# Optimization experiments

Hardware: AMD Instinct MI355X
Metric: run time of the kernel (lower is better)

Reference implementation:

```python
import jax, jax.numpy as jnp
import numpy as np
from jax import lax

# Hyperparameters (mirror init_kwargs)
R = 0.2          # ball-query radius
K = 32           # max neighbors per ball
SPATIAL_STRIDE = 4
TKS = 3          # temporal kernel size (odd)
TSTRIDE = 1
PAD = (1, 1)     # replicate temporal padding


def fps(xyz, m):
    """Furthest point sampling. xyz: (N,3) -> (m,) int32 indices. Starts at index 0."""
    N = xyz.shape[0]

    def body(carry, _):
        dists, last = carry
        d = jnp.sum((xyz - xyz[last]) ** 2, axis=-1)
        dists = jnp.minimum(dists, d)
        nxt = jnp.argmax(dists).astype(jnp.int32)
        return (dists, nxt), nxt

    init = (jnp.full((N,), 1e10, xyz.dtype), jnp.int32(0))
    _, idx = lax.scan(body, init, None, length=m - 1)
    return jnp.concatenate([jnp.zeros((1,), jnp.int32), idx])


def ball_query(pts, anchors):
    """pts: (N,3), anchors: (M,3) -> (M,K) int32. First K indices within radius R,
    padded with the first found index (0 if the ball is empty) -- pointnet2 semantics."""
    N = pts.shape[0]
    d2 = jnp.sum((anchors[:, None, :] - pts[None, :, :]) ** 2, axis=-1)  # (M,N)
    score = jnp.where(d2 < R * R, jnp.arange(N, dtype=jnp.int32)[None, :], N)
    vals, _ = lax.top_k(-score, K)          # ascending first-K valid indices
    sel = -vals                              # (M,K)
    first = sel[:, :1]
    sel = jnp.where(sel >= N, first, sel)    # pad with first in-ball index
    sel = jnp.where(sel >= N, 0, sel)        # empty ball -> index 0
    return sel


def setup_inputs() -> dict:
    key = jax.random.key(0)
    k1, k2, k3, k4, k5 = jax.random.split(key, 5)
    B, T, N, Cin = 4, 8, 4096, 64
    C0, C1 = 64, 128
    xyzs = jax.random.uniform(k1, (B, T, N, 3), dtype=jnp.float32)
    features = jax.random.normal(k2, (B, T, Cin, N), dtype=jnp.float32)
    Wd = jax.random.normal(k3, (C0, 4), dtype=jnp.float32) * 0.1    # conv_d 1x1 weight
    Wf = jax.random.normal(k4, (C0, Cin), dtype=jnp.float32) * 0.1  # conv_f 1x1 weight
    W1 = jax.random.normal(k5, (C1, C0), dtype=jnp.float32) * 0.1   # mlp 1x1 weight
    return {"xyzs": xyzs, "features": features, "Wd": Wd, "Wf": Wf, "W1": W1}


def reference(xyzs, features, Wd, Wf, W1):
    B, T, N, _ = xyzs.shape
    M = N // SPATIAL_STRIDE
    half = TKS // 2
    # replicate temporal padding (PAD = (1,1))
    xp = jnp.concatenate([xyzs[:, :1], xyzs, xyzs[:, -1:]], axis=1)          # (B,L,N,3)
    fp = jnp.concatenate([features[:, :1], features, features[:, -1:]], axis=1)  # (B,L,C,N)
    L = T + PAD[0] + PAD[1]

    new_xyzs, new_feats = [], []
    for t in range(half, L - half, TSTRIDE):
        aidx = jax.vmap(lambda p: fps(p, M))(xp[:, t])                       # (B,M)
        anchor = jnp.take_along_axis(xp[:, t], aidx[:, :, None], axis=1)    # (B,M,3)
        acc = None
        for i in range(t - half, t + half + 1):
            pts = xp[:, i]                                                   # (B,N,3)
            idx = jax.vmap(ball_query)(pts, anchor)                          # (B,M,K)
            grouped = jax.vmap(lambda p, ii: p[ii])(pts, idx)                # (B,M,K,3)
            disp = grouped - anchor[:, :, None, :]
            tcol = jnp.full(disp.shape[:-1] + (1,), float(i - t), disp.dtype)
            d4 = jnp.concatenate([disp, tcol], axis=-1)                      # (B,M,K,4)
            dfeat = jax.nn.relu(jnp.einsum('bmkc,oc->bmko', d4, Wd))         # conv_d
            gf = jax.vmap(lambda f, ii: f.T[ii])(fp[:, i], idx)              # (B,M,K,Cin)
            ffeat = jax.nn.relu(jnp.einsum('bmkc,oc->bmko', gf, Wf))         # conv_f
            feat = ffeat + dfeat                                             # operator '+'
            feat = jax.nn.relu(jnp.einsum('bmkc,oc->bmko', feat, W1))        # mlp
            feat = jnp.max(feat, axis=2)                                     # spatial max -> (B,M,C1)
            acc = feat if acc is None else acc + feat                        # temporal sum
        new_xyzs.append(anchor)
        new_feats.append(jnp.transpose(acc, (0, 2, 1)))                      # (B,C1,M)
    return jnp.stack(new_xyzs, axis=1), jnp.stack(new_feats, axis=1)
```

## Files before the change

kernel.cpp:

```cpp
#include <hip/hip_runtime.h>
#include <hip/hip_bf16.h>

constexpr int B = 4, T = 8, N = 4096, C0 = 64, C1 = 128;
constexpr int M = 1024, KNN = 32;

typedef __attribute__((ext_vector_type(8))) short short8;
typedef __attribute__((ext_vector_type(4))) float f32x4;

__device__ __forceinline__ unsigned short f2bf(float x) {
  unsigned u = __float_as_uint(x);
  u = u + 0x7FFFu + ((u >> 16) & 1u);
  return (unsigned short)(u >> 16);
}
__device__ __forceinline__ float bf2f(unsigned short h) {
  return __uint_as_float((unsigned)h << 16);
}
__device__ __forceinline__ short f2bf_rn(float x) {
  union { __hip_bfloat16 b; unsigned short u; } v;
  v.b = __float2bfloat16(x);
  return (short)v.u;
}

template <int CTRL>
__device__ __forceinline__ float dppf(float x) {
  return __int_as_float(__builtin_amdgcn_update_dpp(0, __float_as_int(x), CTRL, 0xF, 0xF, true));
}
template <int CTRL>
__device__ __forceinline__ int dppi(int x) {
  return __builtin_amdgcn_update_dpp(0, x, CTRL, 0xF, 0xF, true);
}
template <int CTRL>
__device__ __forceinline__ unsigned long long dppu64(unsigned long long x) {
  unsigned lo = (unsigned)dppi<CTRL>((int)(unsigned)x);
  unsigned hi = (unsigned)dppi<CTRL>((int)(unsigned)(x >> 32));
  return ((unsigned long long)hi << 32) | lo;
}
__device__ __forceinline__ void kmerge(unsigned long long& a, unsigned long long b) {
  if (b > a) a = b;
}
__device__ __forceinline__ unsigned long long kmax(unsigned long long a, unsigned long long b) {
  return b > a ? b : a;
}

__global__ __launch_bounds__(256) void prep_wft(const float* __restrict__ Wf,
                                                float* __restrict__ WfT) {
  int t = blockIdx.x * 256 + threadIdx.x;
  if (t < 64 * 64) WfT[t] = Wf[(t & 63) * 64 + (t >> 6)];
}

__global__ __launch_bounds__(256) void prep_w1frag(const float* __restrict__ W1,
                                                   unsigned short* __restrict__ w1hi,
                                                   unsigned short* __restrict__ w1lo) {
  int t = blockIdx.x * 256 + threadIdx.x;
  if (t >= 8192) return;
  int j = t & 7, lane = (t >> 3) & 63, mt = (t >> 9) & 7, kt = t >> 12;
  int row = mt * 16 + (lane & 15);
  int k = kt * 32 + (lane >> 4) * 8 + j;
  float v = W1[row * 64 + k];
  unsigned short hi = f2bf(v);
  w1hi[t] = hi;
  w1lo[t] = f2bf(v - bf2f(hi));
}

__device__ void fps_body(char* smem, const float* __restrict__ xyz,
                         float* __restrict__ out_xyz, int bt) {
  float4* P4 = (float4*)smem;
  int* pick_l = (int*)(smem + 65536);
  unsigned long long* wslot = (unsigned long long*)(smem + 65536 + 4096);
  const float* p = xyz + (size_t)bt * N * 3;
  int tid = threadIdx.x;
  int lane = tid & 63, w = tid >> 6;
  for (int i = tid; i < N; i += 256)
    P4[i] = make_float4(p[i * 3 + 0], p[i * 3 + 1], p[i * 3 + 2], 0.f);
  if (tid == 0) pick_l[0] = 0;
  __syncthreads();
  float X[16], Y[16], Z[16], D[16];
  unsigned inv[16];
#pragma unroll
  for (int j = 0; j < 16; ++j) {
    float4 v = P4[j * 256 + tid];
    X[j] = v.x; Y[j] = v.y; Z[j] = v.z;
    D[j] = 1e10f;
    inv[j] = ~(unsigned)(j * 256 + tid);
  }
  int lidx = 0;
  for (int s = 1; s < M; ++s) {
    float4 lp = P4[lidx];
    unsigned long long k[16];
#pragma unroll
    for (int j = 0; j < 16; ++j) {
      float dx = __fsub_rn(X[j], lp.x);
      float dy = __fsub_rn(Y[j], lp.y);
      float dz = __fsub_rn(Z[j], lp.z);
      float d = __fadd_rn(__fadd_rn(__fmul_rn(dx, dx), __fmul_rn(dy, dy)), __fmul_rn(dz, dz));
      float nd = fminf(D[j], d);
      D[j] = nd;
      k[j] = ((unsigned long long)__float_as_uint(nd) << 32) | inv[j];
    }
#pragma unroll
    for (int st = 8; st >= 1; st >>= 1)
#pragma unroll
      for (int j = 0; j < st; ++j) kmerge(k[j], k[j + st]);
    unsigned long long best = k[0];
    kmerge(best, dppu64<0xB1>(best));
    kmerge(best, dppu64<0x4E>(best));
    kmerge(best, dppu64<0x141>(best));
    kmerge(best, dppu64<0x140>(best));
    int buf = s & 1;
    if ((lane & 15) == 0) wslot[buf * 16 + w * 4 + (lane >> 4)] = best;
    __syncthreads();
    const ulonglong2* ws2 = (const ulonglong2*)&wslot[buf * 16];
    ulonglong2 a0 = ws2[0], a1 = ws2[1], a2 = ws2[2], a3 = ws2[3];
    ulonglong2 a4 = ws2[4], a5 = ws2[5], a6 = ws2[6], a7 = ws2[7];
    unsigned long long t0 = kmax(kmax(a0.x, a0.y), kmax(a1.x, a1.y));
    unsigned long long t1 = kmax(kmax(a2.x, a2.y), kmax(a3.x, a3.y));
    unsigned long long t2 = kmax(kmax(a4.x, a4.y), kmax(a5.x, a5.y));
    unsigned long long t3 = kmax(kmax(a6.x, a6.y), kmax(a7.x, a7.y));
    unsigned long long g = kmax(kmax(t0, t1), kmax(t2, t3));
    lidx = (int)(~(unsigned)g);
    if (tid == 0) pick_l[s] = lidx;
  }
  __syncthreads();
  float* outp = out_xyz + (size_t)bt * M * 3;
  for (int mm = tid; mm < M; mm += 256) {
    float4 v = P4[pick_l[mm]];
    outp[mm * 3 + 0] = v.x;
    outp[mm * 3 + 1] = v.y;
    outp[mm * 3 + 2] = v.z;
  }
}

__device__ void rff_body(char* smem, const float* __restrict__ f,
                         const float* __restrict__ WfT, unsigned short* __restrict__ RFFh,
                         int rid) {
  float (*tile)[65] = (float (*)[65])smem;
  int bt = rid >> 6;
  int n0 = (rid & 63) * 64;
  const float* src = f + (size_t)bt * C0 * N;
  int tx = threadIdx.x & 63, ty = threadIdx.x >> 6;
  for (int r = ty; r < 64; r += 4)
    tile[r][tx] = src[(size_t)r * N + n0 + tx];
  __syncthreads();
  float acc[16];
#pragma unroll
  for (int oo = 0; oo < 16; ++oo) acc[oo] = 0.f;
  int obase = ty * 16;
#pragma unroll 4
  for (int c = 0; c < 64; ++c) {
    float fv = tile[c][tx];
    const float* wr = WfT + c * 64 + obase;
#pragma unroll
    for (int oo = 0; oo < 16; ++oo) acc[oo] = fmaf(fv, wr[oo], acc[oo]);
  }
  __syncthreads();
#pragma unroll
  for (int oo = 0; oo < 16; ++oo) tile[obase + oo][tx] = fmaxf(acc[oo], 0.f);
  __syncthreads();
  unsigned short* dst = RFFh + ((size_t)bt * N + n0) * 64;
  for (int r = ty; r < 64; r += 4)
    dst[(size_t)r * 64 + tx] = f2bf(tile[tx][r]);
}

__global__ __launch_bounds__(256) void fps_rff_kernel(const float* __restrict__ xyz,
                                                      float* __restrict__ out_xyz,
                                                      const float* __restrict__ feats,
                                                      const float* __restrict__ WfT,
                                                      unsigned short* __restrict__ RFFh) {
  __shared__ __align__(16) char smem[65536 + 4096 + 256];
  if (blockIdx.x < 32)
    fps_body(smem, xyz, out_xyz, blockIdx.x);
  else
    rff_body(smem, feats, WfT, RFFh, blockIdx.x - 32);
}

__global__ __launch_bounds__(256) void ballq_kernel(const float* __restrict__ xyz,
                                                    const float* __restrict__ anchors,
                                                    int* __restrict__ idxbuf) {
  const float R2 = 0.04f;
  int w = threadIdx.x >> 6, lane = threadIdx.x & 63;
  int q = blockIdx.x * 4 + w;
  int m = q & (M - 1);
  int di = (q >> 10) % 3;
  int bt = q / (M * 3);
  int b = bt >> 3, t = bt & 7;
  int srct = t + di - 1;
  srct = srct < 0 ? 0 : (srct > 7 ? 7 : srct);
  const float* anc = anchors + ((size_t)(bt * M + m)) * 3;
  float ax = anc[0], ay = anc[1], az = anc[2];
  const float* pts = xyz + ((size_t)(b * T + srct)) * N * 3;
  int* outp = idxbuf + (size_t)q * KNN;
  int cnt = 0, first = 0;
  for (int c = 0; c < N / 64 && cnt < KNN; ++c) {
    int pi = c * 64 + lane;
    const float* pp = pts + (size_t)pi * 3;
    float dx = __fsub_rn(ax, pp[0]);
    float dy = __fsub_rn(ay, pp[1]);
    float dz = __fsub_rn(az, pp[2]);
    float d2 = __fadd_rn(__fadd_rn(__fmul_rn(dx, dx), __fmul_rn(dy, dy)), __fmul_rn(dz, dz));
    bool hit = d2 < R2;
    unsigned long long mask = __ballot(hit);
    if (cnt == 0 && mask) first = c * 64 + (int)__builtin_ctzll(mask);
    int prefix = (int)__popcll(mask & ((1ull << lane) - 1ull));
    int slot = cnt + prefix;
    if (hit && slot < KNN) outp[slot] = pi;
    cnt += (int)__popcll(mask);
  }
  int cntK = cnt < KNN ? cnt : KNN;
  int fill = (cnt == 0) ? 0 : first;
  if (lane < KNN && lane >= cntK) outp[lane] = fill;
}

__global__ __launch_bounds__(256) void mlp_kernel(const float* __restrict__ xyz,
                                                  const unsigned short* __restrict__ RFFh,
                                                  const unsigned short* __restrict__ w1hi,
                                                  const unsigned short* __restrict__ w1lo,
                                                  const float* __restrict__ Wd,
                                                  const float* __restrict__ anchors,
                                                  const int* __restrict__ idxbuf,
                                                  float* __restrict__ out_feats) {
  __shared__ unsigned short Ah[8192];
  __shared__ unsigned short Al[8192];
  __shared__ float wd_l[256];
  __shared__ float fstage[4][128];
  int tid = threadIdx.x;
  {
    uint4* dh = (uint4*)Ah;
    const uint4* sh = (const uint4*)w1hi;
    uint4* dl = (uint4*)Al;
    const uint4* sl = (const uint4*)w1lo;
    for (int i = tid; i < 1024; i += 256) { dh[i] = sh[i]; dl[i] = sl[i]; }
    wd_l[tid] = Wd[tid];
  }
  __syncthreads();
  int w = tid >> 6, lane = tid & 63;
  int nloc = lane & 15, grp = lane >> 4;
  int bid = blockIdx.x;
  int swz = ((bid & 7) << 10) | (bid >> 3);
  int bt = swz >> 8;
  int m0 = (swz & 255) * 4;
  int m = m0 + w;
  int b = bt >> 3, t = bt & 7;
  int aoff = __builtin_amdgcn_readfirstlane(bt * M + m);
  float ax = anchors[(size_t)aoff * 3 + 0];
  float ay = anchors[(size_t)aoff * 3 + 1];
  float az = anchors[(size_t)aoff * 3 + 2];
  f32x4 acc[8];
#pragma unroll
  for (int mt = 0; mt < 8; ++mt) acc[mt] = (f32x4){0.f, 0.f, 0.f, 0.f};

  short8 pg0[2][2], pg1[2][2];
  float ppx[2][2], ppy[2][2], ppz[2][2];

#define MLOADP(BUF, DI)                                                        \
  {                                                                            \
    int srct = t + (DI)-1;                                                     \
    srct = srct < 0 ? 0 : (srct > 7 ? 7 : srct);                               \
    const unsigned short* rf = RFFh + ((size_t)(b * T + srct)) * N * 64;       \
    const float* pts = xyz + ((size_t)(b * T + srct)) * N * 3;                 \
    const int* ip = idxbuf + ((size_t)((bt * 3 + (DI)) * M + m)) * KNN;        \
    int n0 = ip[nloc], n1 = ip[16 + nloc];                                     \
    _Pragma("unroll") for (int kt = 0; kt < 2; ++kt) {                         \
      pg0[BUF][kt] = *(const short8*)(rf + (size_t)n0 * 64 + kt * 32 + grp * 8); \
      pg1[BUF][kt] = *(const short8*)(rf + (size_t)n1 * 64 + kt * 32 + grp * 8); \
    }                                                                          \
    ppx[BUF][0] = pts[n0 * 3 + 0];                                             \
    ppy[BUF][0] = pts[n0 * 3 + 1];                                             \
    ppz[BUF][0] = pts[n0 * 3 + 2];                                             \
    ppx[BUF][1] = pts[n1 * 3 + 0];                                             \
    ppy[BUF][1] = pts[n1 * 3 + 1];                                             \
    ppz[BUF][1] = pts[n1 * 3 + 2];                                             \
  }

#define MCOMPUTE(BUF, DI)                                                      \
  {                                                                            \
    int zro = 0;                                                               \
    asm volatile("" : "+v"(zro));                                              \
    const unsigned short* AhO = Ah + zro;                                      \
    const unsigned short* AlO = Al + zro;                                      \
    const float* wdO = (const float*)wd_l + zro;                               \
    float tvv = (float)((DI)-1);                                               \
    float dx0 = ppx[BUF][0] - ax, dy0 = ppy[BUF][0] - ay, dz0 = ppz[BUF][0] - az; \
    float dx1 = ppx[BUF][1] - ax, dy1 = ppy[BUF][1] - ay, dz1 = ppz[BUF][1] - az; \
    short8 Bh[2][2];                                             \
    _Pragma("unroll") for (int kt = 0; kt < 2; ++kt) {                         \
      short8 bh0, bh1;                                                         \
      _Pragma("unroll") for (int j = 0; j < 8; ++j) {                          \
        int ch = kt * 32 + grp * 8 + j;                                        \
        float4 wr = *(const float4*)&wdO[ch * 4];                              \
        float dd0 = fmaf(dx0, wr.x, fmaf(dy0, wr.y, fmaf(dz0, wr.z, tvv * wr.w))); \
        float dd1 = fmaf(dx1, wr.x, fmaf(dy1, wr.y, fmaf(dz1, wr.z, tvv * wr.w))); \
        float h0 = bf2f((unsigned short)pg0[BUF][kt][j]) + fmaxf(dd0, 0.f);    \
        float h1 = bf2f((unsigned short)pg1[BUF][kt][j]) + fmaxf(dd1, 0.f);    \
        bh0[j] = f2bf_rn(h0);                                                  \
        bh1[j] = f2bf_rn(h1);                                                  \
      }                                                                        \
      Bh[kt][0] = bh0;                                                         \
      Bh[kt][1] = bh1;                                                         \
    }                                                                          \
    _Pragma("unroll") for (int hf = 0; hf < 2; ++hf) {                         \
      f32x4 c[4][2];                                                           \
      _Pragma("unroll") for (int mq = 0; mq < 4; ++mq) {                       \
        c[mq][0] = (f32x4){0.f, 0.f, 0.f, 0.f};                                \
        c[mq][1] = (f32x4){0.f, 0.f, 0.f, 0.f};                                \
      }                                                                        \
      _Pragma("unroll") for (int kt = 0; kt < 2; ++kt) {                       \
        _Pragma("unroll") for (int mq = 0; mq < 4; ++mq) {                     \
          int fo = ((kt * 8 + hf * 4 + mq) * 64 + lane) * 8;                   \
          short8 ahf = *(const short8*)&AhO[fo];                               \
          short8 alf = *(const short8*)&AlO[fo];                               \
          c[mq][0] =                                                           \
              __builtin_amdgcn_mfma_f32_16x16x32_bf16(ahf, Bh[kt][0], c[mq][0], 0, 0, 0); \
          c[mq][0] =                                                           \
              __builtin_amdgcn_mfma_f32_16x16x32_bf16(alf, Bh[kt][0], c[mq][0], 0, 0, 0); \
          c[mq][1] =                                                           \
              __builtin_amdgcn_mfma_f32_16x16x32_bf16(ahf, Bh[kt][1], c[mq][1], 0, 0, 0); \
          c[mq][1] =                                                           \
              __builtin_amdgcn_mfma_f32_16x16x32_bf16(alf, Bh[kt][1], c[mq][1], 0, 0, 0); \
        }                                                                      \
      }                                                                        \
      _Pragma("unroll") for (int mq = 0; mq < 4; ++mq)                         \
          _Pragma("unroll") for (int r = 0; r < 4; ++r) {                      \
        float o = fmaxf(c[mq][0][r], c[mq][1][r]);                             \
        o = fmaxf(o, dppf<0xB1>(o));                                           \
        o = fmaxf(o, dppf<0x4E>(o));                                           \
        o = fmaxf(o, dppf<0x141>(o));                                          \
        o = fmaxf(o, dppf<0x140>(o));                                          \
        acc[hf * 4 + mq][r] += fmaxf(o, 0.f);                                  \
      }                                                                        \
    }                                                                          \
  }

  MLOADP(0, 0)
  MLOADP(1, 1)
  MCOMPUTE(0, 0)
  MLOADP(0, 2)
  MCOMPUTE(1, 1)
  MCOMPUTE(0, 2)
#undef MLOADP
#undef MCOMPUTE

  if (nloc == 0) {
#pragma unroll
    for (int mt = 0; mt < 8; ++mt)
#pragma unroll
      for (int r = 0; r < 4; ++r)
        fstage[w][mt * 16 + grp * 4 + r] = acc[mt][r];
  }
  __syncthreads();
  if (tid < 128) {
    float4 v = make_float4(fstage[0][tid], fstage[1][tid], fstage[2][tid], fstage[3][tid]);
    *(float4*)&out_feats[((size_t)(bt * C1 + tid)) * M + m0] = v;
  }
}

extern "C" void kernel_launch(void* const* d_in, const int* in_sizes, int n_in,
                              void* d_out, int out_size, void* d_ws, size_t ws_size,
                              hipStream_t stream) {
  const float* xyzs = (const float*)d_in[0];
  const float* feats = (const float*)d_in[1];
  const float* Wd = (const float*)d_in[2];
  const float* Wf = (const float*)d_in[3];
  const float* W1 = (const float*)d_in[4];
  float* out_xyz = (float*)d_out;
  float* out_feats = (float*)d_out + (size_t)B * T * M * 3;
  char* ws = (char*)d_ws;
  unsigned short* RFFh = (unsigned short*)ws;
  int* idxbuf = (int*)(ws + (size_t)B * T * N * 64 * 4);
  char* tail = ws + (size_t)B * T * N * 64 * 4 + (size_t)B * T * 3 * M * KNN * 4;
  float* WfT = (float*)tail;
  unsigned short* w1hi = (unsigned short*)(tail + 16384);
  unsigned short* w1lo = (unsigned short*)(tail + 32768);
  prep_wft<<<16, 256, 0, stream>>>(Wf, WfT);
  prep_w1frag<<<32, 256, 0, stream>>>(W1, w1hi, w1lo);
  fps_rff_kernel<<<32 + 2048, 256, 0, stream>>>(xyzs, out_xyz, feats, WfT, RFFh);
  ballq_kernel<<<(B * T * 3 * M) / 4, 256, 0, stream>>>(xyzs, out_xyz, idxbuf);
  mlp_kernel<<<(B * T * M) / 4, 256, 0, stream>>>(xyzs, RFFh, w1hi, w1lo, Wd, out_xyz,
                                                  idxbuf, out_feats);
}
```

Before: 1.056 ms.

## Fuse FPS, ball query and MLP into persistent producer-consumer megakernel

FPS blocks now publish anchors incrementally and bump a per-frame progress counter with release stores. 480 persistent consumer blocks spin on that counter, run the ball query inline into LDS and then do the MLP, so consumers overlap with the serial FPS. This also removes the idxbuf round trip through global memory. RFF moves to its own kernel ahead of the megakernel, and the FPS reduction is trimmed to a full-wave DPP reduction and a 4-slot barrier, which lowers per-iteration sync cost. The risks are spin-wait correctness (it depends on all 32 FPS blocks being co-resident) and reduced consumer parallelism.

```diff
diff --git a/kernel.cpp b/kernel.cpp
--- a/kernel.cpp
+++ b/kernel.cpp
@@ -3,6 +3,9 @@
 
 constexpr int B = 4, T = 8, N = 4096, C0 = 64, C1 = 128;
 constexpr int M = 1024, KNN = 32;
+constexpr int NCONS = 480;
+constexpr int NBLK = 32 + NCONS;
+constexpr int SMEM_BYTES = 49408;
 
 typedef __attribute__((ext_vector_type(8))) short short8;
 typedef __attribute__((ext_vector_type(4))) float f32x4;
@@ -40,6 +43,19 @@
 }
 __device__ __forceinline__ unsigned long long kmax(unsigned long long a, unsigned long long b) {
   return b > a ? b : a;
+}
+
+__device__ __forceinline__ void aStoreF(float* p, float v) {
+  __hip_atomic_store(p, v, __ATOMIC_RELAXED, __HIP_MEMORY_SCOPE_AGENT);
+}
+__device__ __forceinline__ float aLoadF(const float* p) {
+  return __hip_atomic_load(p, __ATOMIC_RELAXED, __HIP_MEMORY_SCOPE_AGENT);
+}
+__device__ __forceinline__ void aStoreRelI(int* p, int v) {
+  __hip_atomic_store(p, v, __ATOMIC_RELEASE, __HIP_MEMORY_SCOPE_AGENT);
+}
+__device__ __forceinline__ int aLoadAcqI(const int* p) {
+  return __hip_atomic_load(p, __ATOMIC_ACQUIRE, __HIP_MEMORY_SCOPE_AGENT);
 }
 
 __global__ __launch_bounds__(256) void prep_wft(const float* __restrict__ Wf,
@@ -62,36 +78,86 @@
   w1lo[t] = f2bf(v - bf2f(hi));
 }
 
+__global__ __launch_bounds__(256) void rff_kernel(const float* __restrict__ f,
+                                                  const float* __restrict__ WfT,
+                                                  unsigned short* __restrict__ RFFh) {
+  __shared__ float tile[64][65];
+  int bt = blockIdx.y;
+  int n0 = blockIdx.x * 64;
+  const float* src = f + (size_t)bt * C0 * N;
+  int tx = threadIdx.x & 63, ty = threadIdx.x >> 6;
+  for (int r = ty; r < 64; r += 4)
+    tile[r][tx] = src[(size_t)r * N + n0 + tx];
+  __syncthreads();
+  float acc[16];
+#pragma unroll
+  for (int oo = 0; oo < 16; ++oo) acc[oo] = 0.f;
+  int obase = ty * 16;
+#pragma unroll 4
+  for (int c = 0; c < 64; ++c) {
+    float fv = tile[c][tx];
+    const float* wr = WfT + c * 64 + obase;
+#pragma unroll
+    for (int oo = 0; oo < 16; ++oo) acc[oo] = fmaf(fv, wr[oo], acc[oo]);
+  }
+  __syncthreads();
+#pragma unroll
+  for (int oo = 0; oo < 16; ++oo) tile[obase + oo][tx] = fmaxf(acc[oo], 0.f);
+  __syncthreads();
+  unsigned short* dst = RFFh + ((size_t)bt * N + n0) * 64;
+  for (int r = ty; r < 64; r += 4)
+    dst[(size_t)r * 64 + tx] = f2bf(tile[tx][r]);
+}
+
 __device__ void fps_body(char* smem, const float* __restrict__ xyz,
-                         float* __restrict__ out_xyz, int bt) {
-  float4* P4 = (float4*)smem;
-  int* pick_l = (int*)(smem + 65536);
-  unsigned long long* wslot = (unsigned long long*)(smem + 65536 + 4096);
+                         float* __restrict__ anchors, int* __restrict__ progress, int bt) {
+  float* xs = (float*)smem;
+  float* ys = xs + N;
+  float* zs = ys + N;
+  unsigned long long* wslot = (unsigned long long*)(smem + 49152);
   const float* p = xyz + (size_t)bt * N * 3;
   int tid = threadIdx.x;
   int lane = tid & 63, w = tid >> 6;
-  for (int i = tid; i < N; i += 256)
-    P4[i] = make_float4(p[i * 3 + 0], p[i * 3 + 1], p[i * 3 + 2], 0.f);
-  if (tid == 0) pick_l[0] = 0;
+  for (int i = tid; i < N; i += 256) {
+    xs[i] = p[i * 3 + 0];
+    ys[i] = p[i * 3 + 1];
+    zs[i] = p[i * 3 + 2];
+  }
   __syncthreads();
   float X[16], Y[16], Z[16], D[16];
   unsigned inv[16];
 #pragma unroll
   for (int j = 0; j < 16; ++j) {
-    float4 v = P4[j * 256 + tid];
-    X[j] = v.x; Y[j] = v.y; Z[j] = v.z;
+    X[j] = xs[j * 256 + tid];
+    Y[j] = ys[j * 256 + tid];
+    Z[j] = zs[j * 256 + tid];
     D[j] = 1e10f;
     inv[j] = ~(unsigned)(j * 256 + tid);
   }
+  if (tid == 0) {
+    float* a0 = anchors + (size_t)bt * M * 3;
+    aStoreF(a0 + 0, xs[0]);
+    aStoreF(a0 + 1, ys[0]);
+    aStoreF(a0 + 2, zs[0]);
+  }
   int lidx = 0;
   for (int s = 1; s < M; ++s) {
-    float4 lp = P4[lidx];
+    float lx = xs[lidx], ly = ys[lidx], lz = zs[lidx];
+    if (tid == 0) {
+      if (s > 1) {
+        float* ap = anchors + ((size_t)(bt * M + s - 1)) * 3;
+        aStoreF(ap + 0, lx);
+        aStoreF(ap + 1, ly);
+        aStoreF(ap + 2, lz);
+      }
+      if ((s & 31) == 0) aStoreRelI(&progress[bt], s);
+    }
     unsigned long long k[16];
 #pragma unroll
     for (int j = 0; j < 16; ++j) {
-      float dx = __fsub_rn(X[j], lp.x);
-      float dy = __fsub_rn(Y[j], lp.y);
-      float dz = __fsub_rn(Z[j], lp.z);
+      float dx = __fsub_rn(X[j], lx);
+      float dy = __fsub_rn(Y[j], ly);
+      float dz = __fsub_rn(Z[j], lz);
       float d = __fadd_rn(__fadd_rn(__fmul_rn(dx, dx), __fmul_rn(dy, dy)), __fmul_rn(dz, dz));
       float nd = fminf(D[j], d);
       D[j] = nd;
@@ -106,89 +172,31 @@
     kmerge(best, dppu64<0x4E>(best));
     kmerge(best, dppu64<0x141>(best));
     kmerge(best, dppu64<0x140>(best));
+    kmerge(best, dppu64<0x142>(best));
+    kmerge(best, dppu64<0x143>(best));
     int buf = s & 1;
-    if ((lane & 15) == 0) wslot[buf * 16 + w * 4 + (lane >> 4)] = best;
-    __syncthreads();
-    const ulonglong2* ws2 = (const ulonglong2*)&wslot[buf * 16];
-    ulonglong2 a0 = ws2[0], a1 = ws2[1], a2 = ws2[2], a3 = ws2[3];
-    ulonglong2 a4 = ws2[4], a5 = ws2[5], a6 = ws2[6], a7 = ws2[7];
-    unsigned long long t0 = kmax(kmax(a0.x, a0.y), kmax(a1.x, a1.y));
-    unsigned long long t1 = kmax(kmax(a2.x, a2.y), kmax(a3.x, a3.y));
-    unsigned long long t2 = kmax(kmax(a4.x, a4.y), kmax(a5.x, a5.y));
-    unsigned long long t3 = kmax(kmax(a6.x, a6.y), kmax(a7.x, a7.y));
-    unsigned long long g = kmax(kmax(t0, t1), kmax(t2, t3));
+    if (lane == 63) wslot[buf * 4 + w] = best;
+    asm volatile("s_waitcnt lgkmcnt(0)" ::: "memory");
+    __builtin_amdgcn_s_barrier();
+    __builtin_amdgcn_sched_barrier(0);
+    const ulonglong2* ws2 = (const ulonglong2*)&wslot[buf * 4];
+    ulonglong2 a0 = ws2[0], a1 = ws2[1];
+    unsigned long long g = kmax(kmax(a0.x, a0.y), kmax(a1.x, a1.y));
     lidx = (int)(~(unsigned)g);
-    if (tid == 0) pick_l[s] = lidx;
-  }
-  __syncthreads();
-  float* outp = out_xyz + (size_t)bt * M * 3;
-  for (int mm = tid; mm < M; mm += 256) {
-    float4 v = P4[pick_l[mm]];
-    outp[mm * 3 + 0] = v.x;
-    outp[mm * 3 + 1] = v.y;
-    outp[mm * 3 + 2] = v.z;
-  }
-}
-
-__device__ void rff_body(char* smem, const float* __restrict__ f,
-                         const float* __restrict__ WfT, unsigned short* __restrict__ RFFh,
-                         int rid) {
-  float (*tile)[65] = (float (*)[65])smem;
-  int bt = rid >> 6;
-  int n0 = (rid & 63) * 64;
-  const float* src = f + (size_t)bt * C0 * N;
-  int tx = threadIdx.x & 63, ty = threadIdx.x >> 6;
-  for (int r = ty; r < 64; r += 4)
-    tile[r][tx] = src[(size_t)r * N + n0 + tx];
-  __syncthreads();
-  float acc[16];
-#pragma unroll
-  for (int oo = 0; oo < 16; ++oo) acc[oo] = 0.f;
-  int obase = ty * 16;
-#pragma unroll 4
-  for (int c = 0; c < 64; ++c) {
-    float fv = tile[c][tx];
-    const float* wr = WfT + c * 64 + obase;
-#pragma unroll
-    for (int oo = 0; oo < 16; ++oo) acc[oo] = fmaf(fv, wr[oo], acc[oo]);
-  }
-  __syncthreads();
-#pragma unroll
-  for (int oo = 0; oo < 16; ++oo) tile[obase + oo][tx] = fmaxf(acc[oo], 0.f);
-  __syncthreads();
-  unsigned short* dst = RFFh + ((size_t)bt * N + n0) * 64;
-  for (int r = ty; r < 64; r += 4)
-    dst[(size_t)r * 64 + tx] = f2bf(tile[tx][r]);
-}
-
-__global__ __launch_bounds__(256) void fps_rff_kernel(const float* __restrict__ xyz,
-                                                      float* __restrict__ out_xyz,
-                                                      const float* __restrict__ feats,
-                                                      const float* __restrict__ WfT,
-                                                      unsigned short* __restrict__ RFFh) {
-  __shared__ __align__(16) char smem[65536 + 4096 + 256];
-  if (blockIdx.x < 32)
-    fps_body(smem, xyz, out_xyz, blockIdx.x);
-  else
-    rff_body(smem, feats, WfT, RFFh, blockIdx.x - 32);
-}
-
-__global__ __launch_bounds__(256) void ballq_kernel(const float* __restrict__ xyz,
-                                                    const float* __restrict__ anchors,
-                                                    int* __restrict__ idxbuf) {
+  }
+  if (tid == 0) {
+    float* ap = anchors + ((size_t)(bt * M + M - 1)) * 3;
+    aStoreF(ap + 0, xs[lidx]);
+    aStoreF(ap + 1, ys[lidx]);
+    aStoreF(ap + 2, zs[lidx]);
+    aStoreRelI(&progress[bt], M);
+  }
+}
+
+__device__ void ballq_one(const float* __restrict__ pts, float ax, float ay, float az,
+                          int* outp) {
   const float R2 = 0.04f;
-  int w = threadIdx.x >> 6, lane = threadIdx.x & 63;
-  int q = blockIdx.x * 4 + w;
-  int m = q & (M - 1);
-  int di = (q >> 10) % 3;
-  int bt = q / (M * 3);
-  int b = bt >> 3, t = bt & 7;
-  int srct = t + di - 1;
-  srct = srct < 0 ? 0 : (srct > 7 ? 7 : srct);
-  const float* anc = anchors + ((size_t)(bt * M + m)) * 3;
-  float ax = anc[0], ay = anc[1], az = anc[2];
-  const float* pts = xyz + ((size_t)(b * T + srct)) * N * 3;
-  int* outp = idxbuf + (size_t)q * KNN;
+  int lane = threadIdx.x & 63;
   int cnt = 0, first = 0;
   for (int c = 0; c < N / 64 && cnt < KNN; ++c) {
     int pi = c * 64 + lane;
@@ -210,19 +218,21 @@
   if (lane < KNN && lane >= cntK) outp[lane] = fill;
 }
 
-__global__ __launch_bounds__(256) void mlp_kernel(const float* __restrict__ xyz,
-                                                  const unsigned short* __restrict__ RFFh,
-                                                  const unsigned short* __restrict__ w1hi,
-                                                  const unsigned short* __restrict__ w1lo,
-                                                  const float* __restrict__ Wd,
-                                                  const float* __restrict__ anchors,
-                                                  const int* __restrict__ idxbuf,
-                                                  float* __restrict__ out_feats) {
-  __shared__ unsigned short Ah[8192];
-  __shared__ unsigned short Al[8192];
-  __shared__ float wd_l[256];
-  __shared__ float fstage[4][128];
+__device__ void consumer_body(char* smem, const float* __restrict__ xyz,
+                              const float* __restrict__ anchors,
+                              const unsigned short* __restrict__ RFFh,
+                              const unsigned short* __restrict__ w1hi,
+                              const unsigned short* __restrict__ w1lo,
+                              const float* __restrict__ Wd,
+                              float* __restrict__ out_feats,
+                              int* __restrict__ progress, int cid) {
   int tid = threadIdx.x;
+  unsigned short* Ah = (unsigned short*)smem;
+  unsigned short* Al = (unsigned short*)(smem + 16384);
+  float* wd_l = (float*)(smem + 32768);
+  float* anc_lds = (float*)(smem + 33792);
+  int* idx_lds = (int*)(smem + 33856);
+  float (*fstage)[128] = (float (*)[128])(smem + 35392);
   {
     uint4* dh = (uint4*)Ah;
     const uint4* sh = (const uint4*)w1hi;
@@ -234,123 +244,159 @@
   __syncthreads();
   int w = tid >> 6, lane = tid & 63;
   int nloc = lane & 15, grp = lane >> 4;
-  int bid = blockIdx.x;
-  int swz = ((bid & 7) << 10) | (bid >> 3);
-  int bt = swz >> 8;
-  int m0 = (swz & 255) * 4;
-  int m = m0 + w;
-  int b = bt >> 3, t = bt & 7;
-  int aoff = __builtin_amdgcn_readfirstlane(bt * M + m);
-  float ax = anchors[(size_t)aoff * 3 + 0];
-  float ay = anchors[(size_t)aoff * 3 + 1];
-  float az = anchors[(size_t)aoff * 3 + 2];
-  f32x4 acc[8];
-#pragma unroll
-  for (int mt = 0; mt < 8; ++mt) acc[mt] = (f32x4){0.f, 0.f, 0.f, 0.f};
-
-  short8 pg0[2][2], pg1[2][2];
-  float ppx[2][2], ppy[2][2], ppz[2][2];
-
-#define MLOADP(BUF, DI)                                                        \
-  {                                                                            \
-    int srct = t + (DI)-1;                                                     \
-    srct = srct < 0 ? 0 : (srct > 7 ? 7 : srct);                               \
-    const unsigned short* rf = RFFh + ((size_t)(b * T + srct)) * N * 64;       \
-    const float* pts = xyz + ((size_t)(b * T + srct)) * N * 3;                 \
-    const int* ip = idxbuf + ((size_t)((bt * 3 + (DI)) * M + m)) * KNN;        \
-    int n0 = ip[nloc], n1 = ip[16 + nloc];                                     \
-    _Pragma("unroll") for (int kt = 0; kt < 2; ++kt) {                         \
+  for (int tile = cid; tile < 8192; tile += NCONS) {
+    int mg = tile >> 5, bt = tile & 31;
+    int m0 = mg * 4;
+    int b = bt >> 3, t = bt & 7;
+    int m = m0 + w;
+    if (tid == 0) {
+      for (int it = 0; it < 1000000 && aLoadAcqI(&progress[bt]) < m0 + 4; ++it)
+        __builtin_amdgcn_s_sleep(8);
+    }
+    __syncthreads();
+    if (lane == 0) {
+      const float* ap = anchors + ((size_t)(bt * M + m)) * 3;
+      anc_lds[w * 4 + 0] = aLoadF(ap + 0);
+      anc_lds[w * 4 + 1] = aLoadF(ap + 1);
+      anc_lds[w * 4 + 2] = aLoadF(ap + 2);
+    }
+    asm volatile("s_waitcnt lgkmcnt(0)" ::: "memory");
+    __builtin_amdgcn_sched_barrier(0);
+    float ax = anc_lds[w * 4 + 0];
+    float ay = anc_lds[w * 4 + 1];
+    float az = anc_lds[w * 4 + 2];
+    for (int di = 0; di < 3; ++di) {
+      int srct = t + di - 1;
+      srct = srct < 0 ? 0 : (srct > 7 ? 7 : srct);
+      ballq_one(xyz + ((size_t)(b * T + srct)) * N * 3, ax, ay, az,
+                idx_lds + (w * 3 + di) * KNN);
+    }
+    asm volatile("s_waitcnt lgkmcnt(0)" ::: "memory");
+    __builtin_amdgcn_sched_barrier(0);
+    f32x4 acc[8];
+#pragma unroll
+    for (int mt = 0; mt < 8; ++mt) acc[mt] = (f32x4){0.f, 0.f, 0.f, 0.f};
+    short8 pg0[2][2], pg1[2][2];
+    float ppx[2][2], ppy[2][2], ppz[2][2];
+
+#define MLOADP(BUF, DI)                                                          \
+  {                                                                              \
+    int srct = t + (DI)-1;                                                       \
+    srct = srct < 0 ? 0 : (srct > 7 ? 7 : srct);                                 \
+    const unsigned short* rf = RFFh + ((size_t)(b * T + srct)) * N * 64;         \
+    const float* pts = xyz + ((size_t)(b * T + srct)) * N * 3;                   \
+    const int* ipw = idx_lds + (w * 3 + (DI)) * KNN;                             \
+    int n0 = ipw[nloc], n1 = ipw[16 + nloc];                                     \
+    _Pragma("unroll") for (int kt = 0; kt < 2; ++kt) {                           \
       pg0[BUF][kt] = *(const short8*)(rf + (size_t)n0 * 64 + kt * 32 + grp * 8); \
       pg1[BUF][kt] = *(const short8*)(rf + (size_t)n1 * 64 + kt * 32 + grp * 8); \
-    }                                                                          \
-    ppx[BUF][0] = pts[n0 * 3 + 0];                                             \
-    ppy[BUF][0] = pts[n0 * 3 + 1];                                             \
-    ppz[BUF][0] = pts[n0 * 3 + 2];                                             \
-    ppx[BUF][1] = pts[n1 * 3 + 0];                                             \
-    ppy[BUF][1] = pts[n1 * 3 + 1];                                             \
-    ppz[BUF][1] = pts[n1 * 3 + 2];                                             \
-  }
-
-#define MCOMPUTE(BUF, DI)                                                      \
-  {                                                                            \
-    int zro = 0;                                                               \
-    asm volatile("" : "+v"(zro));                                              \
-    const unsigned short* AhO = Ah + zro;                                      \
-    const unsigned short* AlO = Al + zro;                                      \
-    const float* wdO = (const float*)wd_l + zro;                               \
-    float tvv = (float)((DI)-1);                                               \
-    float dx0 = ppx[BUF][0] - ax, dy0 = ppy[BUF][0] - ay, dz0 = ppz[BUF][0] - az; \
-    float dx1 = ppx[BUF][1] - ax, dy1 = ppy[BUF][1] - ay, dz1 = ppz[BUF][1] - az; \
-    short8 Bh[2][2];                                             \
-    _Pragma("unroll") for (int kt = 0; kt < 2; ++kt) {                         \
-      short8 bh0, bh1;                                                         \
-      _Pragma("unroll") for (int j = 0; j < 8; ++j) {                          \
-        int ch = kt * 32 + grp * 8 + j;                                        \
-        float4 wr = *(const float4*)&wdO[ch * 4];                              \
+    }                                                                            \
+    ppx[BUF][0] = pts[n0 * 3 + 0];                                               \
+    ppy[BUF][0] = pts[n0 * 3 + 1];                                               \
+    ppz[BUF][0] = pts[n0 * 3 + 2];                                               \
+    ppx[BUF][1] = pts[n1 * 3 + 0];                                               \
+    ppy[BUF][1] = pts[n1 * 3 + 1];                                               \
+    ppz[BUF][1] = pts[n1 * 3 + 2];                                               \
+  }
+
+#define MCOMPUTE(BUF, DI)                                                          \
+  {                                                                                \
+    int zro = 0;                                                                   \
+    asm volatile("" : "+v"(zro));                                                  \
+    const unsigned short* AhO = Ah + zro;                                          \
+    const unsigned short* AlO = Al + zro;                                          \
+    const float* wdO = wd_l + zro;                                                 \
+    float tvv = (float)((DI)-1);                                                   \
+    float dx0 = ppx[BUF][0] - ax, dy0 = ppy[BUF][0] - ay, dz0 = ppz[BUF][0] - az;  \
+    float dx1 = ppx[BUF][1] - ax, dy1 = ppy[BUF][1] - ay, dz1 = ppz[BUF][1] - az;  \
+    short8 Bh[2][2];                                                               \
+    _Pragma("unroll") for (int kt = 0; kt < 2; ++kt) {                             \
+      short8 bh0, bh1;                                                             \
+      _Pragma("unroll") for (int j = 0; j < 8; ++j) {                              \
+        int ch = kt * 32 + grp * 8 + j;                                            \
+        float4 wr = *(const float4*)&wdO[ch * 4];                                  \
         float dd0 = fmaf(dx0, wr.x, fmaf(dy0, wr.y, fmaf(dz0, wr.z, tvv * wr.w))); \
         float dd1 = fmaf(dx1, wr.x, fmaf(dy1, wr.y, fmaf(dz1, wr.z, tvv * wr.w))); \
-        float h0 = bf2f((unsigned short)pg0[BUF][kt][j]) + fmaxf(dd0, 0.f);    \
-        float h1 = bf2f((unsigned short)pg1[BUF][kt][j]) + fmaxf(dd1, 0.f);    \
-        bh0[j] = f2bf_rn(h0);                                                  \
-        bh1[j] = f2bf_rn(h1);                                                  \
-      }                                                                        \
-      Bh[kt][0] = bh0;                                                         \
-      Bh[kt][1] = bh1;                                                         \
-    }                                                                          \
-    _Pragma("unroll") for (int hf = 0; hf < 2; ++hf) {                         \
-      f32x4 c[4][2];                                                           \
-      _Pragma("unroll") for (int mq = 0; mq < 4; ++mq) {                       \
-        c[mq][0] = (f32x4){0.f, 0.f, 0.f, 0.f};                                \
-        c[mq][1] = (f32x4){0.f, 0.f, 0.f, 0.f};                                \
-      }                                                                        \
-      _Pragma("unroll") for (int kt = 0; kt < 2; ++kt) {                       \
-        _Pragma("unroll") for (int mq = 0; mq < 4; ++mq) {                     \
-          int fo = ((kt * 8 + hf * 4 + mq) * 64 + lane) * 8;                   \
-          short8 ahf = *(const short8*)&AhO[fo];                               \
-          short8 alf = *(const short8*)&AlO[fo];                               \
-          c[mq][0] =                                                           \
-              __builtin_amdgcn_mfma_f32_16x16x32_bf16(ahf, Bh[kt][0], c[mq][0], 0, 0, 0); \
-          c[mq][0] =                                                           \
-              __builtin_amdgcn_mfma_f32_16x16x32_bf16(alf, Bh[kt][0], c[mq][0], 0, 0, 0); \
-          c[mq][1] =                                                           \
-              __builtin_amdgcn_mfma_f32_16x16x32_bf16(ahf, Bh[kt][1], c[mq][1], 0, 0, 0); \
-          c[mq][1] =                                                           \
-              __builtin_amdgcn_mfma_f32_16x16x32_bf16(alf, Bh[kt][1], c[mq][1], 0, 0, 0); \
-        }                                                                      \
-      }                                                                        \
-      _Pragma("unroll") for (int mq = 0; mq < 4; ++mq)                         \
-          _Pragma("unroll") for (int r = 0; r < 4; ++r) {                      \
-        float o = fmaxf(c[mq][0][r], c[mq][1][r]);                             \
-        o = fmaxf(o, dppf<0xB1>(o));                                           \
-        o = fmaxf(o, dppf<0x4E>(o));                                           \
-        o = fmaxf(o, dppf<0x141>(o));                                          \
-        o = fmaxf(o, dppf<0x140>(o));                                          \
-        acc[hf * 4 + mq][r] += fmaxf(o, 0.f);                                  \
-      }                                                                        \
-    }                                                                          \
-  }
-
-  MLOADP(0, 0)
-  MLOADP(1, 1)
-  MCOMPUTE(0, 0)
-  MLOADP(0, 2)
-  MCOMPUTE(1, 1)
-  MCOMPUTE(0, 2)
+        float h0 = bf2f((unsigned short)pg0[BUF][kt][j]) + fmaxf(dd0, 0.f);        \
+        float h1 = bf2f((unsigned short)pg1[BUF][kt][j]) + fmaxf(dd1, 0.f);        \
+        bh0[j] = f2bf_rn(h0);                                                      \
+        bh1[j] = f2bf_rn(h1);                                                      \
+      }                                                                            \
+      Bh[kt][0] = bh0;                                                             \
+      Bh[kt][1] = bh1;                                                             \
+    }                                                                              \
+    _Pragma("unroll") for (int hf = 0; hf < 2; ++hf) {                             \
+      f32x4 c[4][2];                                                               \
+      _Pragma("unroll") for (int mq = 0; mq < 4; ++mq) {                           \
+        c[mq][0] = (f32x4){0.f, 0.f, 0.f, 0.f};                                    \
+        c[mq][1] = (f32x4){0.f, 0.f, 0.f, 0.f};                                    \
+      }                                                                            \
+      _Pragma("unroll") for (int kt = 0; kt < 2; ++kt) {                           \
+        _Pragma("unroll") for (int mq = 0; mq < 4; ++mq) {                         \
+          int fo = ((kt * 8 + hf * 4 + mq) * 64 + lane) * 8;                       \
+          short8 ahf = *(const short8*)&AhO[fo];                                   \
+          short8 alf = *(const short8*)&AlO[fo];                                   \
+          c[mq][0] = __builtin_amdgcn_mfma_f32_16x16x32_bf16(ahf, Bh[kt][0],       \
+                                                             c[mq][0], 0, 0, 0);  \
+          c[mq][0] = __builtin_amdgcn_mfma_f32_16x16x32_bf16(alf, Bh[kt][0],       \
+                                                             c[mq][0], 0, 0, 0);  \
+          c[mq][1] = __builtin_amdgcn_mfma_f32_16x16x32_bf16(ahf, Bh[kt][1],       \
+                                                             c[mq][1], 0, 0, 0);  \
+          c[mq][1] = __builtin_amdgcn_mfma_f32_16x16x32_bf16(alf, Bh[kt][1],       \
+                                                             c[mq][1], 0, 0, 0);  \
+        }                                                                          \
+      }                                                                            \
+      _Pragma("unroll") for (int mq = 0; mq < 4; ++mq)                             \
+          _Pragma("unroll") for (int r = 0; r < 4; ++r) {                          \
+        float o = fmaxf(c[mq][0][r], c[mq][1][r]);                                 \
+        o = fmaxf(o, dppf<0xB1>(o));                                               \
+        o = fmaxf(o, dppf<0x4E>(o));                                               \
+        o = fmaxf(o, dppf<0x141>(o));                                              \
+        o = fmaxf(o, dppf<0x140>(o));                                              \
+        acc[hf * 4 + mq][r] += fmaxf(o, 0.f);                                      \
+      }                                                                            \
+    }                                                                              \
+  }
+
+    MLOADP(0, 0)
+    MLOADP(1, 1)
+    MCOMPUTE(0, 0)
+    MLOADP(0, 2)
+    MCOMPUTE(1, 1)
+    MCOMPUTE(0, 2)
 #undef MLOADP
 #undef MCOMPUTE
 
-  if (nloc == 0) {
-#pragma unroll
-    for (int mt = 0; mt < 8; ++mt)
-#pragma unroll
-      for (int r = 0; r < 4; ++r)
-        fstage[w][mt * 16 + grp * 4 + r] = acc[mt][r];
-  }
-  __syncthreads();
-  if (tid < 128) {
-    float4 v = make_float4(fstage[0][tid], fstage[1][tid], fstage[2][tid], fstage[3][tid]);
-    *(float4*)&out_feats[((size_t)(bt * C1 + tid)) * M + m0] = v;
-  }
+    if (nloc == 0) {
+#pragma unroll
+      for (int mt = 0; mt < 8; ++mt)
+#pragma unroll
+        for (int r = 0; r < 4; ++r)
+          fstage[w][mt * 16 + grp * 4 + r] = acc[mt][r];
+    }
+    __syncthreads();
+    if (tid < 128) {
+      float4 v = make_float4(fstage[0][tid], fstage[1][tid], fstage[2][tid], fstage[3][tid]);
+      *(float4*)&out_feats[((size_t)(bt * C1 + tid)) * M + m0] = v;
+    }
+    __syncthreads();
+  }
+}
+
+__global__ __launch_bounds__(256) void mega_kernel(const float* __restrict__ xyz,
+                                                   float* __restrict__ anchors,
+                                                   const unsigned short* __restrict__ RFFh,
+                                                   const unsigned short* __restrict__ w1hi,
+                                                   const unsigned short* __restrict__ w1lo,
+                                                   const float* __restrict__ Wd,
+                                                   float* __restrict__ out_feats,
+                                                   int* __restrict__ progress) {
+  __shared__ __align__(16) char smem[SMEM_BYTES];
+  if (blockIdx.x < 32)
+    fps_body(smem, xyz, anchors, progress, blockIdx.x);
+  else
+    consumer_body(smem, xyz, anchors, RFFh, w1hi, w1lo, Wd, out_feats, progress,
+                  blockIdx.x - 32);
 }
 
 extern "C" void kernel_launch(void* const* d_in, const int* in_sizes, int n_in,
@@ -365,15 +411,15 @@
   float* out_feats = (float*)d_out + (size_t)B * T * M * 3;
   char* ws = (char*)d_ws;
   unsigned short* RFFh = (unsigned short*)ws;
-  int* idxbuf = (int*)(ws + (size_t)B * T * N * 64 * 4);
-  char* tail = ws + (size_t)B * T * N * 64 * 4 + (size_t)B * T * 3 * M * KNN * 4;
+  char* tail = ws + (size_t)B * T * N * 64 * 2;
   float* WfT = (float*)tail;
   unsigned short* w1hi = (unsigned short*)(tail + 16384);
   unsigned short* w1lo = (unsigned short*)(tail + 32768);
+  int* progress = (int*)(tail + 49152);
+  hipMemsetAsync(progress, 0, 128, stream);
   prep_wft<<<16, 256, 0, stream>>>(Wf, WfT);
   prep_w1frag<<<32, 256, 0, stream>>>(W1, w1hi, w1lo);
-  fps_rff_kernel<<<32 + 2048, 256, 0, stream>>>(xyzs, out_xyz, feats, WfT, RFFh);
-  ballq_kernel<<<(B * T * 3 * M) / 4, 256, 0, stream>>>(xyzs, out_xyz, idxbuf);
-  mlp_kernel<<<(B * T * M) / 4, 256, 0, stream>>>(xyzs, RFFh, w1hi, w1lo, Wd, out_xyz,
-                                                  idxbuf, out_feats);
-}
+  rff_kernel<<<dim3(N / 64, B * T), 256, 0, stream>>>(feats, WfT, RFFh);
+  mega_kernel<<<NBLK, 256, 0, stream>>>(xyzs, out_xyz, RFFh, w1hi, w1lo, Wd, out_feats,
+                                        progress);
+}
```

New measurement: 1.293 ms. 1.22x slower.

## Speed up FPS loop with packed math, wave-wide reduction and lighter barrier

Applied to the files above, without the earlier changes.

The FPS distance update now uses two-wide float vectors so the compiler can emit packed FP32 ops, and point coordinates move to SoA shared arrays. Each wave finishes its argmax with extra row-broadcast DPP steps so only one lane per wave writes to LDS. The block sync becomes a raw s_barrier with a waitcnt, which cuts the per-iteration cross-wave reduction from 16 slots to 4. Picked anchors are written straight to global memory inside the loop, and the LDS footprint and workspace offset are shrunk. FPS is a serial chain of 1023 steps, so per-step latency matters; the raw barrier gives up the compiler's fence guarantees, and fp contract is disabled to keep rounding identical.

```diff
diff --git a/kernel.cpp b/kernel.cpp
--- a/kernel.cpp
+++ b/kernel.cpp
@@ -6,6 +6,7 @@
 
 typedef __attribute__((ext_vector_type(8))) short short8;
 typedef __attribute__((ext_vector_type(4))) float f32x4;
+typedef __attribute__((ext_vector_type(2))) float f32x2;
 
 __device__ __forceinline__ unsigned short f2bf(float x) {
   unsigned u = __float_as_uint(x);
@@ -64,38 +65,55 @@
 
 __device__ void fps_body(char* smem, const float* __restrict__ xyz,
                          float* __restrict__ out_xyz, int bt) {
-  float4* P4 = (float4*)smem;
-  int* pick_l = (int*)(smem + 65536);
-  unsigned long long* wslot = (unsigned long long*)(smem + 65536 + 4096);
+#pragma clang fp contract(off)
+  float* xs = (float*)smem;
+  float* ys = xs + N;
+  float* zs = ys + N;
+  unsigned long long* wslot = (unsigned long long*)(smem + 49152);
   const float* p = xyz + (size_t)bt * N * 3;
   int tid = threadIdx.x;
   int lane = tid & 63, w = tid >> 6;
-  for (int i = tid; i < N; i += 256)
-    P4[i] = make_float4(p[i * 3 + 0], p[i * 3 + 1], p[i * 3 + 2], 0.f);
-  if (tid == 0) pick_l[0] = 0;
-  __syncthreads();
-  float X[16], Y[16], Z[16], D[16];
+  for (int i = tid; i < N; i += 256) {
+    xs[i] = p[i * 3 + 0];
+    ys[i] = p[i * 3 + 1];
+    zs[i] = p[i * 3 + 2];
+  }
+  __syncthreads();
+  f32x2 X2[8], Y2[8], Z2[8], D2[8];
   unsigned inv[16];
 #pragma unroll
-  for (int j = 0; j < 16; ++j) {
-    float4 v = P4[j * 256 + tid];
-    X[j] = v.x; Y[j] = v.y; Z[j] = v.z;
-    D[j] = 1e10f;
-    inv[j] = ~(unsigned)(j * 256 + tid);
+  for (int j = 0; j < 8; ++j) {
+    int i0 = (2 * j) * 256 + tid, i1 = (2 * j + 1) * 256 + tid;
+    X2[j] = (f32x2){xs[i0], xs[i1]};
+    Y2[j] = (f32x2){ys[i0], ys[i1]};
+    Z2[j] = (f32x2){zs[i0], zs[i1]};
+    D2[j] = (f32x2){1e10f, 1e10f};
+    inv[2 * j] = ~(unsigned)i0;
+    inv[2 * j + 1] = ~(unsigned)i1;
+  }
+  if (tid == 0) {
+    float* a0 = out_xyz + (size_t)bt * M * 3;
+    a0[0] = xs[0]; a0[1] = ys[0]; a0[2] = zs[0];
   }
   int lidx = 0;
   for (int s = 1; s < M; ++s) {
-    float4 lp = P4[lidx];
+    float lx = xs[lidx], ly = ys[lidx], lz = zs[lidx];
+    if (tid == 0 && s > 1) {
+      float* ap = out_xyz + ((size_t)(bt * M + s - 1)) * 3;
+      ap[0] = lx; ap[1] = ly; ap[2] = lz;
+    }
+    f32x2 l2x = (f32x2){lx, lx}, l2y = (f32x2){ly, ly}, l2z = (f32x2){lz, lz};
     unsigned long long k[16];
 #pragma unroll
-    for (int j = 0; j < 16; ++j) {
-      float dx = __fsub_rn(X[j], lp.x);
-      float dy = __fsub_rn(Y[j], lp.y);
-      float dz = __fsub_rn(Z[j], lp.z);
-      float d = __fadd_rn(__fadd_rn(__fmul_rn(dx, dx), __fmul_rn(dy, dy)), __fmul_rn(dz, dz));
-      float nd = fminf(D[j], d);
-      D[j] = nd;
-      k[j] = ((unsigned long long)__float_as_uint(nd) << 32) | inv[j];
+    for (int j = 0; j < 8; ++j) {
+      f32x2 dx = X2[j] - l2x;
+      f32x2 dy = Y2[j] - l2y;
+      f32x2 dz = Z2[j] - l2z;
+      f32x2 d = dx * dx + dy * dy + dz * dz;
+      f32x2 nd = __builtin_elementwise_min(D2[j], d);
+      D2[j] = nd;
+      k[2 * j] = ((unsigned long long)__float_as_uint(nd.x) << 32) | inv[2 * j];
+      k[2 * j + 1] = ((unsigned long long)__float_as_uint(nd.y) << 32) | inv[2 * j + 1];
     }
 #pragma unroll
     for (int st = 8; st >= 1; st >>= 1)
@@ -106,27 +124,21 @@
     kmerge(best, dppu64<0x4E>(best));
     kmerge(best, dppu64<0x141>(best));
     kmerge(best, dppu64<0x140>(best));
+    kmerge(best, dppu64<0x142>(best));
+    kmerge(best, dppu64<0x143>(best));
     int buf = s & 1;
-    if ((lane & 15) == 0) wslot[buf * 16 + w * 4 + (lane >> 4)] = best;
-    __syncthreads();
-    const ulonglong2* ws2 = (const ulonglong2*)&wslot[buf * 16];
-    ulonglong2 a0 = ws2[0], a1 = ws2[1], a2 = ws2[2], a3 = ws2[3];
-    ulonglong2 a4 = ws2[4], a5 = ws2[5], a6 = ws2[6], a7 = ws2[7];
-    unsigned long long t0 = kmax(kmax(a0.x, a0.y), kmax(a1.x, a1.y));
-    unsigned long long t1 = kmax(kmax(a2.x, a2.y), kmax(a3.x, a3.y));
-    unsigned long long t2 = kmax(kmax(a4.x, a4.y), kmax(a5.x, a5.y));
-    unsigned long long t3 = kmax(kmax(a6.x, a6.y), kmax(a7.x, a7.y));
-    unsigned long long g = kmax(kmax(t0, t1), kmax(t2, t3));
+    if (lane == 63) wslot[buf * 4 + w] = best;
+    asm volatile("s_waitcnt lgkmcnt(0)" ::: "memory");
+    __builtin_amdgcn_s_barrier();
+    __builtin_amdgcn_sched_barrier(0);
+    const ulonglong2* ws2 = (const ulonglong2*)&wslot[buf * 4];
+    ulonglong2 a0 = ws2[0], a1 = ws2[1];
+    unsigned long long g = kmax(kmax(a0.x, a0.y), kmax(a1.x, a1.y));
     lidx = (int)(~(unsigned)g);
-    if (tid == 0) pick_l[s] = lidx;
-  }
-  __syncthreads();
-  float* outp = out_xyz + (size_t)bt * M * 3;
-  for (int mm = tid; mm < M; mm += 256) {
-    float4 v = P4[pick_l[mm]];
-    outp[mm * 3 + 0] = v.x;
-    outp[mm * 3 + 1] = v.y;
-    outp[mm * 3 + 2] = v.z;
+  }
+  if (tid == 0) {
+    float* ap = out_xyz + ((size_t)(bt * M + M - 1)) * 3;
+    ap[0] = xs[lidx]; ap[1] = ys[lidx]; ap[2] = zs[lidx];
   }
 }
 
@@ -166,7 +178,7 @@
                                                       const float* __restrict__ feats,
                                                       const float* __restrict__ WfT,
                                                       unsigned short* __restrict__ RFFh) {
-  __shared__ __align__(16) char smem[65536 + 4096 + 256];
+  __shared__ __align__(16) char smem[49152 + 256];
   if (blockIdx.x < 32)
     fps_body(smem, xyz, out_xyz, blockIdx.x);
   else
@@ -365,8 +377,8 @@
   float* out_feats = (float*)d_out + (size_t)B * T * M * 3;
   char* ws = (char*)d_ws;
   unsigned short* RFFh = (unsigned short*)ws;
-  int* idxbuf = (int*)(ws + (size_t)B * T * N * 64 * 4);
-  char* tail = ws + (size_t)B * T * N * 64 * 4 + (size_t)B * T * 3 * M * KNN * 4;
+  int* idxbuf = (int*)(ws + (size_t)B * T * N * 64 * 2);
+  char* tail = ws + (size_t)B * T * N * 64 * 2 + (size_t)B * T * 3 * M * KNN * 4;
   float* WfT = (float*)tail;
   unsigned short* w1hi = (unsigned short*)(tail + 16384);
   unsigned short* w1lo = (unsigned short*)(tail + 32768);
```

New measurement: 928.9 us. 12.1% less time.
